# Performance work log

Measured on AMD Instinct MI355X. Metric: run time of the kernel, lower is better.

Reference implementation:

```python
import jax, jax.numpy as jnp
import numpy as np

DIM, DEPTH, HEADS, DIM_HEAD, MLP = 768, 6, 12, 64, 3072
INNER = HEADS * DIM_HEAD
B, N = 8, 1024
SCALE = DIM_HEAD ** -0.5
EPS = 1e-5


def _ln(x, g, b):
    m = jnp.mean(x, -1, keepdims=True)
    v = jnp.mean(jnp.square(x - m), -1, keepdims=True)
    return (x - m) * jax.lax.rsqrt(v + EPS) * g + b


def _ternary(w):
    # BitNet-style ternary quant with straight-through estimator
    s = jnp.mean(jnp.abs(w)) + 1e-8
    wq = jnp.clip(jnp.round(w / s), -1.0, 1.0) * s
    return w + jax.lax.stop_gradient(wq - w)


def setup_inputs() -> dict:
    key = jax.random.key(0)
    ks = jax.random.split(key, 8)
    d = {
        'x': jax.random.normal(ks[0], (B, N, DIM), jnp.float32),
        'ln1_g': jnp.ones((DEPTH, DIM), jnp.float32),
        'ln1_b': jnp.zeros((DEPTH, DIM), jnp.float32),
        'Wqkv': jax.random.normal(ks[1], (DEPTH, 3 * INNER, DIM), jnp.float32) * 0.02,
        'ln2_g': jnp.ones((DEPTH, INNER), jnp.float32),
        'ln2_b': jnp.zeros((DEPTH, INNER), jnp.float32),
        'Wo': jax.random.normal(ks[2], (DEPTH, DIM, INNER), jnp.float32) * 0.02,
        'bo': jnp.zeros((DEPTH, DIM), jnp.float32),
        'ffln1_g': jnp.ones((DEPTH, DIM), jnp.float32),
        'ffln1_b': jnp.zeros((DEPTH, DIM), jnp.float32),
        'W1': jax.random.normal(ks[3], (DEPTH, MLP, DIM), jnp.float32) * 0.02,
        'b1': jnp.zeros((DEPTH, MLP), jnp.float32),
        'ffln2_g': jnp.ones((DEPTH, MLP), jnp.float32),
        'ffln2_b': jnp.zeros((DEPTH, MLP), jnp.float32),
        'W2': jax.random.normal(ks[4], (DEPTH, DIM, MLP), jnp.float32) * 0.02,
        'b2': jnp.zeros((DEPTH, DIM), jnp.float32),
    }
    return d


def _forward(x, ln1_g, ln1_b, Wqkv, ln2_g, ln2_b, Wo, bo,
             ffln1_g, ffln1_b, W1, b1, ffln2_g, ffln2_b, W2, b2):
    depth = Wqkv.shape[0]
    # layers 0..depth-2 ternary, last layer plain linear
    flag = jnp.concatenate([jnp.ones((depth - 1,), x.dtype), jnp.zeros((1,), x.dtype)])

    def block(h, p):
        (g1, b1n, wqkv, g2, b2n, wo, bo_, fg1, fb1, w1, bb1, fg2, fb2, w2, bb2, f) = p

        def mt(w):
            return f * _ternary(w) + (1.0 - f) * w

        y = _ln(h, g1, b1n)
        qkv = jnp.einsum('bnd,ed->bne', y, mt(wqkv))  # [B,N,3*INNER]
        q, k, v = jnp.split(qkv, 3, axis=-1)
        def heads(t):
            return t.reshape(B, N, HEADS, DIM_HEAD).transpose(0, 2, 1, 3)
        q, k, v = heads(q), heads(k), heads(v)
        attn = jax.nn.softmax(jnp.einsum('bhnd,bhmd->bhnm', q, k) * SCALE, axis=-1)
        o = jnp.einsum('bhnm,bhmd->bhnd', attn, v)
        o = o.transpose(0, 2, 1, 3).reshape(B, N, INNER)
        o = _ln(o, g2, b2n)
        o = jnp.einsum('bne,de->bnd', o, mt(wo)) + bo_
        h = h + o
        y = _ln(h, fg1, fb1)
        y = jnp.einsum('bnd,md->bnm', y, mt(w1)) + bb1
        y = jax.nn.gelu(y, approximate=False)
        y = _ln(y, fg2, fb2)
        y = jnp.einsum('bnm,dm->bnd', y, mt(w2)) + bb2
        return h + y, None

    xs = (ln1_g, ln1_b, Wqkv, ln2_g, ln2_b, Wo, bo,
          ffln1_g, ffln1_b, W1, b1, ffln2_g, ffln2_b, W2, b2, flag)
    out, _ = jax.lax.scan(block, x, xs)
    return out


def reference(x, ln1_g, ln1_b, Wqkv, ln2_g, ln2_b, Wo, bo,
              ffln1_g, ffln1_b, W1, b1, ffln2_g, ffln2_b, W2, b2):
    return _forward(x, ln1_g, ln1_b, Wqkv, ln2_g, ln2_b, Wo, bo,
                    ffln1_g, ffln1_b, W1, b1, ffln2_g, ffln2_b, W2, b2)
```

## Files before the change

### kernel.cpp

```cpp
#include <hip/hip_runtime.h>
#include <hip/hip_bf16.h>
#include <math.h>

typedef __bf16 bf16_t;
typedef __bf16 bf16x4 __attribute__((ext_vector_type(4)));
typedef __bf16 bf16x8 __attribute__((ext_vector_type(8)));
typedef float  f32x4  __attribute__((ext_vector_type(4)));

#define TOKENS 8192
#define DIMV   768
#define INNERV 768
#define QKVW   2304
#define MLPW   3072
#define NSEQ   1024
#define NB     8
#define NH     12
#define DH     64

enum { EP_STORE = 0, EP_BIAS_RES = 1, EP_BIAS_GELU = 2 };

__device__ __forceinline__ void gload_lds16(const bf16_t* g, bf16_t* l)
{
  __builtin_amdgcn_global_load_lds((const __attribute__((address_space(1))) void*)g,
                                   (__attribute__((address_space(3))) void*)l,
                                   16, 0, 0);
}

__global__ __launch_bounds__(256)
void gemm_nt(const bf16_t* __restrict__ A, const bf16_t* __restrict__ B,
             const int K, const int N, const int mode,
             const float* __restrict__ sacc_p, const float sinvn, const float sbias,
             const float* __restrict__ bias,
             float* __restrict__ resid,
             bf16_t* __restrict__ outb,
             float* __restrict__ fout)
{
  __shared__ __align__(16) bf16_t lsA[2][128 * 32];
  __shared__ __align__(16) bf16_t lsB[2][128 * 32];
  const int tid  = threadIdx.x;
  const int lane = tid & 63;
  const int wave = tid >> 6;
  const int wm = wave >> 1, wn = wave & 1;
  const int bm = blockIdx.x, bn = blockIdx.y;

  const int srow = wave * 32 + (lane >> 2);
  const int fsw  = (srow >> 1) & 3;
  const int scol = ((lane & 3) ^ fsw) * 8;
  const bf16_t* gA = A + (size_t)(bm * 128 + srow) * K + scol;
  const bf16_t* gB = B + (size_t)(bn * 128 + srow) * K + scol;
  const int l0 = srow * 32 + (lane & 3) * 8;
  const int l1 = (srow + 16) * 32 + (lane & 3) * 8;

  f32x4 acc[4][4];
#pragma unroll
  for (int i = 0; i < 4; i++)
#pragma unroll
    for (int j = 0; j < 4; j++) acc[i][j] = (f32x4){0.f, 0.f, 0.f, 0.f};

  const int fr   = ((lane & 15) >> 1) & 3;
  const int rsl  = ((lane >> 4) ^ fr) * 8;
  const int arow = (wm * 64 + (lane & 15)) * 32 + rsl;
  const int brow = (wn * 64 + (lane & 15)) * 32 + rsl;

  auto stage = [&](int b, int kb) {
    gload_lds16(gA + kb,                  &lsA[b][l0]);
    gload_lds16(gA + (size_t)16 * K + kb, &lsA[b][l1]);
    gload_lds16(gB + kb,                  &lsB[b][l0]);
    gload_lds16(gB + (size_t)16 * K + kb, &lsB[b][l1]);
  };
  auto compute = [&](int b) {
    bf16x8 af[4], bfv[4];
#pragma unroll
    for (int i = 0; i < 4; i++) af[i]  = *(const bf16x8*)&lsA[b][arow + i * 16 * 32];
#pragma unroll
    for (int j = 0; j < 4; j++) bfv[j] = *(const bf16x8*)&lsB[b][brow + j * 16 * 32];
#pragma unroll
    for (int i = 0; i < 4; i++)
#pragma unroll
      for (int j = 0; j < 4; j++)
        acc[i][j] = __builtin_amdgcn_mfma_f32_16x16x32_bf16(af[i], bfv[j], acc[i][j], 0, 0, 0);
  };

  const int NT = K / 32;
  stage(0, 0);
  stage(1, 32);
  int cur = 0;
  for (int t = 0; t < NT - 1; ++t) {
    asm volatile("s_waitcnt vmcnt(4)" ::: "memory");
    __builtin_amdgcn_s_barrier();
    __builtin_amdgcn_sched_barrier(0);
    compute(cur);
    asm volatile("s_waitcnt lgkmcnt(0)" ::: "memory");
    __builtin_amdgcn_s_barrier();
    __builtin_amdgcn_sched_barrier(0);
    if (t + 2 < NT) stage(cur, (t + 2) * 32);
    cur ^= 1;
  }
  asm volatile("s_waitcnt vmcnt(0)" ::: "memory");
  __builtin_amdgcn_s_barrier();
  __builtin_amdgcn_sched_barrier(0);
  compute(cur);

  const float s = (*sacc_p) * sinvn + sbias;
  const int r0 = bm * 128 + wm * 64 + (lane >> 4) * 4;
  const int c0 = bn * 128 + wn * 64 + (lane & 15);
#pragma unroll
  for (int i = 0; i < 4; i++) {
#pragma unroll
    for (int j = 0; j < 4; j++) {
      const int col = c0 + j * 16;
#pragma unroll
      for (int r = 0; r < 4; r++) {
        const int row = r0 + i * 16 + r;
        const float v = acc[i][j][r] * s;
        const size_t idx = (size_t)row * N + col;
        if (mode == EP_STORE) {
          outb[idx] = (bf16_t)v;
        } else if (mode == EP_BIAS_RES) {
          const float add = v + bias[col];
          if (fout) fout[idx] = resid[idx] + add;
          else      resid[idx] += add;
        } else {
          const float t = v + bias[col];
          outb[idx] = (bf16_t)(0.5f * t * (1.0f + erff(t * 0.70710678118654752f)));
        }
      }
    }
  }
}

template <typename TIN>
__global__ __launch_bounds__(256)
void ln_kern(const TIN* __restrict__ x, const float* __restrict__ g,
             const float* __restrict__ b, bf16_t* __restrict__ y, const int W)
{
  const int row = blockIdx.x;
  const int tid = threadIdx.x;
  const TIN* xr = x + (size_t)row * W;
  float s = 0.f, s2 = 0.f;
  if constexpr (sizeof(TIN) == 4) {
    const f32x4* xv = (const f32x4*)xr;
    for (int i = tid; i < W / 4; i += 256) {
      f32x4 v = xv[i];
#pragma unroll
      for (int e = 0; e < 4; e++) { s += v[e]; s2 += v[e] * v[e]; }
    }
  } else {
    const bf16x8* xv = (const bf16x8*)xr;
    for (int i = tid; i < W / 8; i += 256) {
      bf16x8 v = xv[i];
#pragma unroll
      for (int e = 0; e < 8; e++) { const float f = (float)v[e]; s += f; s2 += f * f; }
    }
  }
#pragma unroll
  for (int off = 32; off > 0; off >>= 1) {
    s  += __shfl_xor(s,  off, 64);
    s2 += __shfl_xor(s2, off, 64);
  }
  __shared__ float red[8];
  if ((tid & 63) == 0) { red[(tid >> 6) * 2] = s; red[(tid >> 6) * 2 + 1] = s2; }
  __syncthreads();
  const float ts  = red[0] + red[2] + red[4] + red[6];
  const float ts2 = red[1] + red[3] + red[5] + red[7];
  const float invW = 1.0f / (float)W;
  const float mean = ts * invW;
  const float var  = fmaxf(ts2 * invW - mean * mean, 0.f);
  const float rs   = rsqrtf(var + 1e-5f);
  bf16_t* yr = y + (size_t)row * W;
  const f32x4* gv = (const f32x4*)g;
  const f32x4* bv = (const f32x4*)b;
  if constexpr (sizeof(TIN) == 4) {
    const f32x4* xv = (const f32x4*)xr;
    bf16x4* yv = (bf16x4*)yr;
    for (int i = tid; i < W / 4; i += 256) {
      f32x4 v = xv[i], gg = gv[i], bb = bv[i];
      bf16x4 o;
#pragma unroll
      for (int e = 0; e < 4; e++) o[e] = (bf16_t)((v[e] - mean) * rs * gg[e] + bb[e]);
      yv[i] = o;
    }
  } else {
    const bf16x8* xv = (const bf16x8*)xr;
    bf16x8* yv = (bf16x8*)yr;
    for (int i = tid; i < W / 8; i += 256) {
      bf16x8 v = xv[i];
      f32x4 g0 = gv[2 * i], g1 = gv[2 * i + 1];
      f32x4 b0 = bv[2 * i], b1 = bv[2 * i + 1];
      bf16x8 o;
#pragma unroll
      for (int e = 0; e < 4; e++) o[e]     = (bf16_t)(((float)v[e]     - mean) * rs * g0[e] + b0[e]);
#pragma unroll
      for (int e = 0; e < 4; e++) o[e + 4] = (bf16_t)(((float)v[e + 4] - mean) * rs * g1[e] + b1[e]);
      yv[i] = o;
    }
  }
}

__global__ __launch_bounds__(256)
void attn_mfma(const bf16_t* __restrict__ qkv, bf16_t* __restrict__ o)
{
  __shared__ __align__(16) bf16_t Ks[64][72];
  __shared__ __align__(16) bf16_t Vt[64][72];
  __shared__ __align__(16) bf16_t Pw[4][16][72];
  const int tid  = threadIdx.x;
  const int lane = tid & 63;
  const int wave = tid >> 6;
  const int quad = lane >> 4;
  const int l15  = lane & 15;
  const int qb = blockIdx.x, hh = blockIdx.y, bb = blockIdx.z;
  const size_t tokbase = (size_t)bb * NSEQ;

  const int qrow = qb * 64 + wave * 16 + l15;
  bf16x8 qf[2];
  {
    const bf16_t* qp = qkv + (tokbase + qrow) * QKVW + hh * DH;
    qf[0] = *(const bf16x8*)(qp + quad * 8);
    qf[1] = *(const bf16x8*)(qp + 32 + quad * 8);
  }

  f32x4 Ot[4];
#pragma unroll
  for (int i = 0; i < 4; i++) Ot[i] = (f32x4){0.f, 0.f, 0.f, 0.f};
  float m_r[4], l_r[4];
#pragma unroll
  for (int r = 0; r < 4; r++) { m_r[r] = -1e30f; l_r[r] = 0.f; }

  const int skv = tid & 63;
  const int sd  = (tid >> 6) * 16;

  bf16x8 k0, k1, v0, v1;
  {
    const bf16_t* kp = qkv + (tokbase + skv) * QKVW + INNERV + hh * DH + sd;
    k0 = *(const bf16x8*)kp;
    k1 = *(const bf16x8*)(kp + 8);
    v0 = *(const bf16x8*)(kp + INNERV);
    v1 = *(const bf16x8*)(kp + INNERV + 8);
  }

  for (int kt = 0; kt < NSEQ / 64; ++kt) {
    __syncthreads();
    *(bf16x8*)&Ks[skv][sd]     = k0;
    *(bf16x8*)&Ks[skv][sd + 8] = k1;
#pragma unroll
    for (int e = 0; e < 8; e++) { Vt[sd + e][skv] = v0[e]; Vt[sd + 8 + e][skv] = v1[e]; }
    __syncthreads();

    bf16x8 nk0 = k0, nk1 = k1, nv0 = v0, nv1 = v1;
    if (kt + 1 < NSEQ / 64) {
      const bf16_t* kp = qkv + (tokbase + (kt + 1) * 64 + skv) * QKVW + INNERV + hh * DH + sd;
      nk0 = *(const bf16x8*)kp;
      nk1 = *(const bf16x8*)(kp + 8);
      nv0 = *(const bf16x8*)(kp + INNERV);
      nv1 = *(const bf16x8*)(kp + INNERV + 8);
    }

    f32x4 st[4];
#pragma unroll
    for (int nt = 0; nt < 4; nt++) {
      bf16x8 b0 = *(const bf16x8*)&Ks[nt * 16 + l15][quad * 8];
      bf16x8 b1 = *(const bf16x8*)&Ks[nt * 16 + l15][32 + quad * 8];
      f32x4 c = (f32x4){0.f, 0.f, 0.f, 0.f};
      c = __builtin_amdgcn_mfma_f32_16x16x32_bf16(qf[0], b0, c, 0, 0, 0);
      c = __builtin_amdgcn_mfma_f32_16x16x32_bf16(qf[1], b1, c, 0, 0, 0);
      st[nt] = c;
    }

    float rmax[4];
#pragma unroll
    for (int r = 0; r < 4; r++) {
      float v = fmaxf(fmaxf(st[0][r], st[1][r]), fmaxf(st[2][r], st[3][r]));
      v = fmaxf(v, __shfl_xor(v, 1, 64));
      v = fmaxf(v, __shfl_xor(v, 2, 64));
      v = fmaxf(v, __shfl_xor(v, 4, 64));
      v = fmaxf(v, __shfl_xor(v, 8, 64));
      rmax[r] = v * 0.125f;
    }
    float alpha[4];
#pragma unroll
    for (int r = 0; r < 4; r++) {
      const float mnew = fmaxf(m_r[r], rmax[r]);
      alpha[r] = __expf(m_r[r] - mnew);
      m_r[r] = mnew;
    }
    float rsum[4] = {0.f, 0.f, 0.f, 0.f};
#pragma unroll
    for (int nt = 0; nt < 4; nt++) {
#pragma unroll
      for (int r = 0; r < 4; r++) {
        const float p = __expf(st[nt][r] * 0.125f - m_r[r]);
        rsum[r] += p;
        Pw[wave][quad * 4 + r][nt * 16 + l15] = (bf16_t)p;
      }
    }
#pragma unroll
    for (int r = 0; r < 4; r++) {
      float v = rsum[r];
      v += __shfl_xor(v, 1, 64);
      v += __shfl_xor(v, 2, 64);
      v += __shfl_xor(v, 4, 64);
      v += __shfl_xor(v, 8, 64);
      l_r[r] = l_r[r] * alpha[r] + v;
    }
#pragma unroll
    for (int dt = 0; dt < 4; dt++)
#pragma unroll
      for (int r = 0; r < 4; r++) Ot[dt][r] *= alpha[r];

    asm volatile("s_waitcnt lgkmcnt(0)" ::: "memory");
    __builtin_amdgcn_sched_barrier(0);

#pragma unroll
    for (int kk = 0; kk < 2; kk++) {
      bf16x8 pa = *(const bf16x8*)&Pw[wave][l15][kk * 32 + quad * 8];
#pragma unroll
      for (int dt = 0; dt < 4; dt++) {
        bf16x8 vb = *(const bf16x8*)&Vt[dt * 16 + l15][kk * 32 + quad * 8];
        Ot[dt] = __builtin_amdgcn_mfma_f32_16x16x32_bf16(pa, vb, Ot[dt], 0, 0, 0);
      }
    }

    k0 = nk0; k1 = nk1; v0 = nv0; v1 = nv1;
  }

  float inv[4];
#pragma unroll
  for (int r = 0; r < 4; r++) inv[r] = 1.0f / l_r[r];
#pragma unroll
  for (int dt = 0; dt < 4; dt++) {
#pragma unroll
    for (int r = 0; r < 4; r++) {
      const int q = qb * 64 + wave * 16 + quad * 4 + r;
      const int d = dt * 16 + l15;
      o[(tokbase + q) * INNERV + hh * DH + d] = (bf16_t)(Ot[dt][r] * inv[r]);
    }
  }
}

__global__ __launch_bounds__(64)
void zero_kern(float* __restrict__ p)
{
  p[threadIdx.x] = 0.f;
}

__global__ __launch_bounds__(256)
void absmean4_kern(const float* __restrict__ w0, const float* __restrict__ w1,
                   const float* __restrict__ w2, const float* __restrict__ w3,
                   const long n0, const long n1, const long n2, const long n3,
                   float* __restrict__ acc)
{
  const int t = blockIdx.y;
  const float* w = (t == 0) ? w0 : (t == 1) ? w1 : (t == 2) ? w2 : w3;
  const long  n  = (t == 0) ? n0 : (t == 1) ? n1 : (t == 2) ? n2 : n3;
  const int tid = threadIdx.x;
  float s = 0.f;
  const size_t stride = (size_t)256 * gridDim.x * 4;
  for (size_t i = ((size_t)blockIdx.x * 256 + tid) * 4; i < (size_t)n; i += stride) {
    f32x4 v = *(const f32x4*)(w + i);
    s += fabsf(v[0]) + fabsf(v[1]) + fabsf(v[2]) + fabsf(v[3]);
  }
#pragma unroll
  for (int off = 32; off > 0; off >>= 1) s += __shfl_xor(s, off, 64);
  __shared__ float red[4];
  if ((tid & 63) == 0) red[tid >> 6] = s;
  __syncthreads();
  if (tid == 0) atomicAdd(&acc[t], red[0] + red[1] + red[2] + red[3]);
}

__global__ __launch_bounds__(256)
void quant4_kern(const float* __restrict__ w0, const float* __restrict__ w1,
                 const float* __restrict__ w2, const float* __restrict__ w3,
                 bf16_t* __restrict__ q0, bf16_t* __restrict__ q1,
                 bf16_t* __restrict__ q2, bf16_t* __restrict__ q3,
                 const int n40, const int n41, const int n42, const int n43,
                 const float* __restrict__ acc,
                 const float inv0, const float inv1, const float inv2, const float inv3)
{
  const int t = blockIdx.y;
  const float* w = (t == 0) ? w0 : (t == 1) ? w1 : (t == 2) ? w2 : w3;
  bf16_t*      q = (t == 0) ? q0 : (t == 1) ? q1 : (t == 2) ? q2 : q3;
  const int   n4 = (t == 0) ? n40 : (t == 1) ? n41 : (t == 2) ? n42 : n43;
  const float iv = (t == 0) ? inv0 : (t == 1) ? inv1 : (t == 2) ? inv2 : inv3;
  const int i = blockIdx.x * 256 + threadIdx.x;
  if (i >= n4) return;
  const float s = acc[t] * iv + 1e-8f;
  f32x4 v = ((const f32x4*)w)[i];
  bf16x4 o;
#pragma unroll
  for (int e = 0; e < 4; e++) {
    float qv = rintf(v[e] / s);
    qv = fminf(1.f, fmaxf(-1.f, qv));
    o[e] = (bf16_t)qv;
  }
  ((bf16x4*)q)[i] = o;
}

__global__ __launch_bounds__(256)
void cast4_kern(const float* __restrict__ w0, const float* __restrict__ w1,
                const float* __restrict__ w2, const float* __restrict__ w3,
                bf16_t* __restrict__ q0, bf16_t* __restrict__ q1,
                bf16_t* __restrict__ q2, bf16_t* __restrict__ q3,
                const int n40, const int n41, const int n42, const int n43)
{
  const int t = blockIdx.y;
  const float* w = (t == 0) ? w0 : (t == 1) ? w1 : (t == 2) ? w2 : w3;
  bf16_t*      q = (t == 0) ? q0 : (t == 1) ? q1 : (t == 2) ? q2 : q3;
  const int   n4 = (t == 0) ? n40 : (t == 1) ? n41 : (t == 2) ? n42 : n43;
  const int i = blockIdx.x * 256 + threadIdx.x;
  if (i >= n4) return;
  f32x4 v = ((const f32x4*)w)[i];
  bf16x4 o;
#pragma unroll
  for (int e = 0; e < 4; e++) o[e] = (bf16_t)v[e];
  ((bf16x4*)q)[i] = o;
}

__global__ __launch_bounds__(256)
void copyf_kern(const float* __restrict__ in, float* __restrict__ out, const int n4)
{
  const int i = blockIdx.x * 256 + threadIdx.x;
  if (i < n4) ((f32x4*)out)[i] = ((const f32x4*)in)[i];
}

extern "C" void kernel_launch(void* const* d_in, const int* in_sizes, int n_in,
                              void* d_out, int out_size, void* d_ws, size_t ws_size,
                              hipStream_t stream)
{
  const float* x     = (const float*)d_in[0];
  const float* ln1_g = (const float*)d_in[1];
  const float* ln1_b = (const float*)d_in[2];
  const float* Wqkv  = (const float*)d_in[3];
  const float* ln2_g = (const float*)d_in[4];
  const float* ln2_b = (const float*)d_in[5];
  const float* Wo    = (const float*)d_in[6];
  const float* bo    = (const float*)d_in[7];
  const float* fg1   = (const float*)d_in[8];
  const float* fb1   = (const float*)d_in[9];
  const float* W1    = (const float*)d_in[10];
  const float* b1    = (const float*)d_in[11];
  const float* fg2   = (const float*)d_in[12];
  const float* fb2   = (const float*)d_in[13];
  const float* W2    = (const float*)d_in[14];
  const float* b2    = (const float*)d_in[15];

  char* ws = (char*)d_ws;
  size_t off = 0;
  float*  sacc  = (float*)(ws + off);  off += 256;
  float*  h     = (float*)(ws + off);  off += (size_t)TOKENS * DIMV * 4;
  bf16_t* bigA  = (bf16_t*)(ws + off); off += (size_t)TOKENS * MLPW * 2;
  bf16_t* bigB  = (bf16_t*)(ws + off); off += (size_t)TOKENS * MLPW * 2;
  bf16_t* q_qkv = (bf16_t*)(ws + off); off += (size_t)QKVW * DIMV * 2;
  bf16_t* q_o   = (bf16_t*)(ws + off); off += (size_t)DIMV * INNERV * 2;
  bf16_t* q_1   = (bf16_t*)(ws + off); off += (size_t)MLPW * DIMV * 2;
  bf16_t* q_2   = (bf16_t*)(ws + off); off += (size_t)DIMV * MLPW * 2;

  bf16_t* obuf   = bigA;
  bf16_t* ln2out = bigA + (size_t)TOKENS * INNERV;

  zero_kern<<<1, 64, 0, stream>>>(sacc);
  copyf_kern<<<TOKENS * DIMV / 4 / 256, 256, 0, stream>>>(x, h, TOKENS * DIMV / 4);

  for (int lyr = 0; lyr < 6; ++lyr) {
    const float* wqkv_l = Wqkv + (size_t)lyr * QKVW * DIMV;
    const float* wo_l   = Wo   + (size_t)lyr * DIMV * INNERV;
    const float* w1_l   = W1   + (size_t)lyr * MLPW * DIMV;
    const float* w2_l   = W2   + (size_t)lyr * DIMV * MLPW;
    const float *sq, *so, *s1, *s2p;
    float iq, io, i1, i2, bq, bo2, bb1v, bb2v;
    if (lyr < 5) {
      absmean4_kern<<<dim3(64, 4), 256, 0, stream>>>(
          wqkv_l, wo_l, w1_l, w2_l,
          (long)QKVW * DIMV, (long)DIMV * INNERV, (long)MLPW * DIMV, (long)DIMV * MLPW,
          &sacc[lyr * 4]);
      quant4_kern<<<dim3(MLPW * DIMV / 1024, 4), 256, 0, stream>>>(
          wqkv_l, wo_l, w1_l, w2_l, q_qkv, q_o, q_1, q_2,
          QKVW * DIMV / 4, DIMV * INNERV / 4, MLPW * DIMV / 4, DIMV * MLPW / 4,
          &sacc[lyr * 4],
          1.0f / (QKVW * DIMV), 1.0f / (DIMV * INNERV), 1.0f / (MLPW * DIMV), 1.0f / (DIMV * MLPW));
      sq = &sacc[lyr * 4 + 0]; iq = 1.0f / (QKVW * DIMV); bq = 1e-8f;
      so = &sacc[lyr * 4 + 1]; io = 1.0f / (DIMV * INNERV); bo2 = 1e-8f;
      s1 = &sacc[lyr * 4 + 2]; i1 = 1.0f / (MLPW * DIMV); bb1v = 1e-8f;
      s2p = &sacc[lyr * 4 + 3]; i2 = 1.0f / (DIMV * MLPW); bb2v = 1e-8f;
    } else {
      cast4_kern<<<dim3(MLPW * DIMV / 1024, 4), 256, 0, stream>>>(
          wqkv_l, wo_l, w1_l, w2_l, q_qkv, q_o, q_1, q_2,
          QKVW * DIMV / 4, DIMV * INNERV / 4, MLPW * DIMV / 4, DIMV * MLPW / 4);
      sq = so = s1 = s2p = &sacc[63];
      iq = io = i1 = i2 = 0.f;
      bq = bo2 = bb1v = bb2v = 1.0f;
    }

    ln_kern<float><<<TOKENS, 256, 0, stream>>>(h, ln1_g + lyr * DIMV, ln1_b + lyr * DIMV, bigA, DIMV);
    gemm_nt<<<dim3(64, QKVW / 128), 256, 0, stream>>>(bigA, q_qkv, DIMV, QKVW, EP_STORE, sq, iq, bq, nullptr, nullptr, bigB, nullptr);
    attn_mfma<<<dim3(NSEQ / 64, NH, NB), 256, 0, stream>>>(bigB, obuf);
    ln_kern<bf16_t><<<TOKENS, 256, 0, stream>>>(obuf, ln2_g + lyr * INNERV, ln2_b + lyr * INNERV, ln2out, INNERV);
    gemm_nt<<<dim3(64, DIMV / 128), 256, 0, stream>>>(ln2out, q_o, INNERV, DIMV, EP_BIAS_RES, so, io, bo2, bo + lyr * DIMV, h, nullptr, nullptr);
    ln_kern<float><<<TOKENS, 256, 0, stream>>>(h, fg1 + lyr * DIMV, fb1 + lyr * DIMV, bigA, DIMV);
    gemm_nt<<<dim3(64, MLPW / 128), 256, 0, stream>>>(bigA, q_1, DIMV, MLPW, EP_BIAS_GELU, s1, i1, bb1v, b1 + lyr * MLPW, nullptr, bigB, nullptr);
    ln_kern<bf16_t><<<TOKENS, 256, 0, stream>>>(bigB, fg2 + lyr * MLPW, fb2 + lyr * MLPW, bigA, MLPW);
    gemm_nt<<<dim3(64, DIMV / 128), 256, 0, stream>>>(bigA, q_2, MLPW, DIMV, EP_BIAS_RES, s2p, i2, bb2v, b2 + lyr * DIMV, h, nullptr,
                                                      (lyr == 5) ? (float*)d_out : nullptr);
  }
}
```

Baseline: 2.591 ms.

## Streamline online softmax in attention with exp2, lazy rescale, deferred row-sum

```diff
diff --git a/kernel.cpp b/kernel.cpp
--- a/kernel.cpp
+++ b/kernel.cpp
@@ -203,6 +203,7 @@
   __shared__ __align__(16) bf16_t Ks[64][72];
   __shared__ __align__(16) bf16_t Vt[64][72];
   __shared__ __align__(16) bf16_t Pw[4][16][72];
+  const float SCL = 0.125f * 1.44269504088896f;
   const int tid  = threadIdx.x;
   const int lane = tid & 63;
   const int wave = tid >> 6;
@@ -222,9 +223,9 @@
   f32x4 Ot[4];
 #pragma unroll
   for (int i = 0; i < 4; i++) Ot[i] = (f32x4){0.f, 0.f, 0.f, 0.f};
-  float m_r[4], l_r[4];
-#pragma unroll
-  for (int r = 0; r < 4; r++) { m_r[r] = -1e30f; l_r[r] = 0.f; }
+  float m2[4], lp[4];
+#pragma unroll
+  for (int r = 0; r < 4; r++) { m2[r] = -1e30f; lp[r] = 0.f; }
 
   const int skv = tid & 63;
   const int sd  = (tid >> 6) * 16;
@@ -256,6 +257,7 @@
     }
 
     f32x4 st[4];
+    __builtin_amdgcn_s_setprio(1);
 #pragma unroll
     for (int nt = 0; nt < 4; nt++) {
       bf16x8 b0 = *(const bf16x8*)&Ks[nt * 16 + l15][quad * 8];
@@ -265,8 +267,9 @@
       c = __builtin_amdgcn_mfma_f32_16x16x32_bf16(qf[1], b1, c, 0, 0, 0);
       st[nt] = c;
     }
-
-    float rmax[4];
+    __builtin_amdgcn_s_setprio(0);
+
+    float rmax2[4];
 #pragma unroll
     for (int r = 0; r < 4; r++) {
       float v = fmaxf(fmaxf(st[0][r], st[1][r]), fmaxf(st[2][r], st[3][r]));
@@ -274,42 +277,35 @@
       v = fmaxf(v, __shfl_xor(v, 2, 64));
       v = fmaxf(v, __shfl_xor(v, 4, 64));
       v = fmaxf(v, __shfl_xor(v, 8, 64));
-      rmax[r] = v * 0.125f;
-    }
-    float alpha[4];
-#pragma unroll
-    for (int r = 0; r < 4; r++) {
-      const float mnew = fmaxf(m_r[r], rmax[r]);
-      alpha[r] = __expf(m_r[r] - mnew);
-      m_r[r] = mnew;
-    }
-    float rsum[4] = {0.f, 0.f, 0.f, 0.f};
+      rmax2[r] = v * SCL;
+    }
+    const bool ok = (rmax2[0] <= m2[0] + 8.f) && (rmax2[1] <= m2[1] + 8.f) &&
+                    (rmax2[2] <= m2[2] + 8.f) && (rmax2[3] <= m2[3] + 8.f);
+    if (!__all(ok)) {
+#pragma unroll
+      for (int r = 0; r < 4; r++) {
+        const float mnew = fmaxf(m2[r], rmax2[r]);
+        const float alpha = exp2f(m2[r] - mnew);
+        m2[r] = mnew;
+        lp[r] *= alpha;
+#pragma unroll
+        for (int dt = 0; dt < 4; dt++) Ot[dt][r] *= alpha;
+      }
+    }
 #pragma unroll
     for (int nt = 0; nt < 4; nt++) {
 #pragma unroll
       for (int r = 0; r < 4; r++) {
-        const float p = __expf(st[nt][r] * 0.125f - m_r[r]);
-        rsum[r] += p;
+        const float p = exp2f(fmaf(st[nt][r], SCL, -m2[r]));
+        lp[r] += p;
         Pw[wave][quad * 4 + r][nt * 16 + l15] = (bf16_t)p;
       }
     }
-#pragma unroll
-    for (int r = 0; r < 4; r++) {
-      float v = rsum[r];
-      v += __shfl_xor(v, 1, 64);
-      v += __shfl_xor(v, 2, 64);
-      v += __shfl_xor(v, 4, 64);
-      v += __shfl_xor(v, 8, 64);
-      l_r[r] = l_r[r] * alpha[r] + v;
-    }
-#pragma unroll
-    for (int dt = 0; dt < 4; dt++)
-#pragma unroll
-      for (int r = 0; r < 4; r++) Ot[dt][r] *= alpha[r];
 
     asm volatile("s_waitcnt lgkmcnt(0)" ::: "memory");
     __builtin_amdgcn_sched_barrier(0);
 
+    __builtin_amdgcn_s_setprio(1);
 #pragma unroll
     for (int kk = 0; kk < 2; kk++) {
       bf16x8 pa = *(const bf16x8*)&Pw[wave][l15][kk * 32 + quad * 8];
@@ -319,13 +315,21 @@
         Ot[dt] = __builtin_amdgcn_mfma_f32_16x16x32_bf16(pa, vb, Ot[dt], 0, 0, 0);
       }
     }
+    __builtin_amdgcn_s_setprio(0);
 
     k0 = nk0; k1 = nk1; v0 = nv0; v1 = nv1;
   }
 
   float inv[4];
 #pragma unroll
-  for (int r = 0; r < 4; r++) inv[r] = 1.0f / l_r[r];
+  for (int r = 0; r < 4; r++) {
+    float v = lp[r];
+    v += __shfl_xor(v, 1, 64);
+    v += __shfl_xor(v, 2, 64);
+    v += __shfl_xor(v, 4, 64);
+    v += __shfl_xor(v, 8, 64);
+    inv[r] = 1.0f / v;
+  }
 #pragma unroll
   for (int dt = 0; dt < 4; dt++) {
 #pragma unroll
```

New measurement: 2.534 ms. -2.2%, faster.
